# Kernel optimization log

Measured on AMD Instinct MI355X. Metric: run time of the kernel, lower is better.

## Reference

```python
import jax, jax.numpy as jnp
import numpy as np

B, L, ENC, DEC, ATT = 128, 196, 2048, 512, 512

def setup_inputs() -> dict:
    key = jax.random.key(0)
    ks = jax.random.split(key, 8)
    s_enc = 1.0 / np.sqrt(ENC)
    s_dec = 1.0 / np.sqrt(DEC)
    s_att = 1.0 / np.sqrt(ATT)
    return {
        "encoder_out": jax.random.normal(ks[0], (B, L, ENC), jnp.float32),
        "decoder_hidden": jax.random.normal(ks[1], (B, DEC), jnp.float32),
        "We": jax.random.uniform(ks[2], (ENC, ATT), jnp.float32, -s_enc, s_enc),
        "be": jax.random.uniform(ks[3], (ATT,), jnp.float32, -s_enc, s_enc),
        "Wd": jax.random.uniform(ks[4], (DEC, ATT), jnp.float32, -s_dec, s_dec),
        "bd": jax.random.uniform(ks[5], (ATT,), jnp.float32, -s_dec, s_dec),
        "wa": jax.random.uniform(ks[6], (ATT,), jnp.float32, -s_att, s_att),
        "ba": jax.random.uniform(ks[7], (), jnp.float32, -s_att, s_att),
    }

def reference(encoder_out, decoder_hidden, We, be, Wd, bd, wa, ba):
    # encoder_out: [B, L, ENC]; decoder_hidden: [B, DEC]
    enc_map = jnp.einsum('ble,ea->bla', encoder_out, We) + be          # [B, L, A]
    dec_map = decoder_hidden @ Wd + bd                                  # [B, A]
    scores = jnp.tanh(enc_map + dec_map[:, None, :]) @ wa + ba         # [B, L]
    alphas = jax.nn.softmax(scores, axis=1)                             # [B, L]
    context = jnp.einsum('bl,ble->be', alphas, encoder_out)             # [B, ENC]
    return (context, alphas)
```

## Files before the change

### kernel.cpp

```cpp
#include <hip/hip_runtime.h>

#define B_   128
#define L_   196
#define ENC_ 2048
#define DEC_ 512
#define ATT_ 512
#define M_   (B_ * L_)

typedef _Float16 f16x4 __attribute__((ext_vector_type(4)));
typedef _Float16 f16x8 __attribute__((ext_vector_type(8)));
typedef __fp16   h16x2 __attribute__((ext_vector_type(2)));
typedef float    f32x4 __attribute__((ext_vector_type(4)));

#define FENCE_LDS_BARRIER()                                        \
    do {                                                           \
        asm volatile("s_waitcnt lgkmcnt(0)" ::: "memory");         \
        __builtin_amdgcn_s_barrier();                              \
        __builtin_amdgcn_sched_barrier(0);                         \
    } while (0)


__global__ void wets_kernel(const float* __restrict__ We, _Float16* __restrict__ WeTs) {
    int u = blockIdx.x * 256 + threadIdx.x;
    int row = u & 127;
    int k8  = (u >> 7) & 3;
    int kt  = (u >> 9) & 63;
    int nt  = u >> 15;
    int n  = nt * 128 + row;
    int k0 = kt * 32 + k8 * 8;
    f16x8 h;
#pragma unroll
    for (int j = 0; j < 8; ++j) h[j] = (_Float16)We[(k0 + j) * ATT_ + n];
    *reinterpret_cast<f16x8*>(WeTs + (size_t)u * 8) = h;
}

__global__ void decmap_kernel(const float* __restrict__ dh, const float* __restrict__ Wd,
                              const float* __restrict__ bd, float* __restrict__ dec) {
    int b = blockIdx.x;
    int a = threadIdx.x;
    float acc = bd[a];
    const float* dhp = dh + b * DEC_;
#pragma unroll 8
    for (int k = 0; k < DEC_; ++k) acc += dhp[k] * Wd[k * ATT_ + a];
    dec[b * ATT_ + a] = acc;
}

__global__ __launch_bounds__(256, 3)
void gemm_score_kernel(const float* __restrict__ enc,
                       const _Float16* __restrict__ WeTs,
                       const float* __restrict__ be,
                       const float* __restrict__ wa,
                       const float* __restrict__ dec,
                       float* __restrict__ partial) {
    __shared__ _Float16 smem[2][2][4096];
    __shared__ float red[2][128];

    int bid = blockIdx.x;
    int sid = (bid & 7) * 98 + (bid >> 3);
    int mtile = sid >> 2;
    int ntile = sid & 3;

    int tid  = threadIdx.x;
    int lane = tid & 63, wid = tid >> 6;
    int wm = wid >> 1, wn = wid & 1;
    int l15 = lane & 15, lg = lane >> 4;

    int arowi = tid >> 2;
    int ac8   = tid & 3;
    const float* agA = enc + (size_t)(mtile * 128 + arowi) * ENC_ + ac8 * 8;
    const float* agB = agA + (size_t)64 * ENC_;
    int wa0 = (ac8 * 128 + (arowi ^ (2 * ac8))) * 8;
    int wa1 = wa0 + 64 * 8;

    const _Float16* bbase = WeTs + (size_t)ntile * 64 * 4096;

    int afo = (lg * 128 + wm * 64 + (l15 ^ (2 * lg))) * 8;
    int bfo = (lg * 128 + wn * 64 + l15) * 8;

    float4 areg0[4], areg1[4];
    f16x8  breg0[2], breg1[2];

    f32x4 acc[4][4];
#pragma unroll
    for (int mi = 0; mi < 4; ++mi)
#pragma unroll
        for (int ni = 0; ni < 4; ++ni) acc[mi][ni] = (f32x4){0.f, 0.f, 0.f, 0.f};

    auto load0 = [&](int kt) {
        const float* a0 = agA + kt * 32;
        const float* a1 = agB + kt * 32;
        areg0[0] = *reinterpret_cast<const float4*>(a0);
        areg0[1] = *reinterpret_cast<const float4*>(a0 + 4);
        areg0[2] = *reinterpret_cast<const float4*>(a1);
        areg0[3] = *reinterpret_cast<const float4*>(a1 + 4);
        const _Float16* bs = bbase + (size_t)kt * 4096;
        breg0[0] = *reinterpret_cast<const f16x8*>(bs + tid * 8);
        breg0[1] = *reinterpret_cast<const f16x8*>(bs + (tid + 256) * 8);
    };
    auto load1 = [&](int kt) {
        const float* a0 = agA + kt * 32;
        const float* a1 = agB + kt * 32;
        areg1[0] = *reinterpret_cast<const float4*>(a0);
        areg1[1] = *reinterpret_cast<const float4*>(a0 + 4);
        areg1[2] = *reinterpret_cast<const float4*>(a1);
        areg1[3] = *reinterpret_cast<const float4*>(a1 + 4);
        const _Float16* bs = bbase + (size_t)kt * 4096;
        breg1[0] = *reinterpret_cast<const f16x8*>(bs + tid * 8);
        breg1[1] = *reinterpret_cast<const f16x8*>(bs + (tid + 256) * 8);
    };
    auto write0 = [&](int buf) {
        _Float16* As = smem[buf][0];
        _Float16* Bs = smem[buf][1];
        union { h16x2 h2[4]; f16x8 h8; } cv;
        cv.h2[0] = __builtin_amdgcn_cvt_pkrtz(areg0[0].x, areg0[0].y);
        cv.h2[1] = __builtin_amdgcn_cvt_pkrtz(areg0[0].z, areg0[0].w);
        cv.h2[2] = __builtin_amdgcn_cvt_pkrtz(areg0[1].x, areg0[1].y);
        cv.h2[3] = __builtin_amdgcn_cvt_pkrtz(areg0[1].z, areg0[1].w);
        *reinterpret_cast<f16x8*>(As + wa0) = cv.h8;
        cv.h2[0] = __builtin_amdgcn_cvt_pkrtz(areg0[2].x, areg0[2].y);
        cv.h2[1] = __builtin_amdgcn_cvt_pkrtz(areg0[2].z, areg0[2].w);
        cv.h2[2] = __builtin_amdgcn_cvt_pkrtz(areg0[3].x, areg0[3].y);
        cv.h2[3] = __builtin_amdgcn_cvt_pkrtz(areg0[3].z, areg0[3].w);
        *reinterpret_cast<f16x8*>(As + wa1) = cv.h8;
        *reinterpret_cast<f16x8*>(Bs + tid * 8) = breg0[0];
        *reinterpret_cast<f16x8*>(Bs + (tid + 256) * 8) = breg0[1];
    };
    auto write1 = [&](int buf) {
        _Float16* As = smem[buf][0];
        _Float16* Bs = smem[buf][1];
        union { h16x2 h2[4]; f16x8 h8; } cv;
        cv.h2[0] = __builtin_amdgcn_cvt_pkrtz(areg1[0].x, areg1[0].y);
        cv.h2[1] = __builtin_amdgcn_cvt_pkrtz(areg1[0].z, areg1[0].w);
        cv.h2[2] = __builtin_amdgcn_cvt_pkrtz(areg1[1].x, areg1[1].y);
        cv.h2[3] = __builtin_amdgcn_cvt_pkrtz(areg1[1].z, areg1[1].w);
        *reinterpret_cast<f16x8*>(As + wa0) = cv.h8;
        cv.h2[0] = __builtin_amdgcn_cvt_pkrtz(areg1[2].x, areg1[2].y);
        cv.h2[1] = __builtin_amdgcn_cvt_pkrtz(areg1[2].z, areg1[2].w);
        cv.h2[2] = __builtin_amdgcn_cvt_pkrtz(areg1[3].x, areg1[3].y);
        cv.h2[3] = __builtin_amdgcn_cvt_pkrtz(areg1[3].z, areg1[3].w);
        *reinterpret_cast<f16x8*>(As + wa1) = cv.h8;
        *reinterpret_cast<f16x8*>(Bs + tid * 8) = breg1[0];
        *reinterpret_cast<f16x8*>(Bs + (tid + 256) * 8) = breg1[1];
    };
    auto compute = [&](const _Float16* As, const _Float16* Bs) {
        f16x8 af[4], bf[4];
#pragma unroll
        for (int mi = 0; mi < 4; ++mi)
            af[mi] = *reinterpret_cast<const f16x8*>(As + afo + mi * 128);
#pragma unroll
        for (int ni = 0; ni < 4; ++ni)
            bf[ni] = *reinterpret_cast<const f16x8*>(Bs + bfo + ni * 128);
#pragma unroll
        for (int mi = 0; mi < 4; ++mi)
#pragma unroll
            for (int ni = 0; ni < 4; ++ni)
                acc[mi][ni] = __builtin_amdgcn_mfma_f32_16x16x32_f16(
                    af[mi], bf[ni], acc[mi][ni], 0, 0, 0);
    };

    load0(0);
    load1(1);
    write0(0);
    FENCE_LDS_BARRIER();

    for (int kt2 = 0; kt2 < 32; ++kt2) {
        int kt = kt2 * 2;
        if (kt2 < 31) load0(kt + 2);
        compute(smem[0][0], smem[0][1]);
        write1(1);
        FENCE_LDS_BARRIER();
        if (kt2 < 31) load1(kt + 3);
        compute(smem[1][0], smem[1][1]);
        if (kt2 < 31) write0(0);
        FENCE_LDS_BARRIER();
    }

    float rsum[4][4];
#pragma unroll
    for (int mi = 0; mi < 4; ++mi)
#pragma unroll
        for (int j = 0; j < 4; ++j) rsum[mi][j] = 0.f;

    int nb = ntile * 128 + wn * 64;
    int rb = mtile * 128 + wm * 64;
#pragma unroll
    for (int ni = 0; ni < 4; ++ni) {
        int n = nb + ni * 16 + l15;
        float wav = wa[n];
        float bev = be[n];
#pragma unroll
        for (int mi = 0; mi < 4; ++mi) {
#pragma unroll
            for (int j = 0; j < 4; ++j) {
                int row = rb + mi * 16 + lg * 4 + j;
                int b = row / L_;
                float x = acc[mi][ni][j] + bev + dec[b * ATT_ + n];
                float e = __expf(2.0f * x);
                float t = 1.0f - 2.0f / (e + 1.0f);
                rsum[mi][j] += t * wav;
            }
        }
    }
#pragma unroll
    for (int mi = 0; mi < 4; ++mi) {
#pragma unroll
        for (int j = 0; j < 4; ++j) {
            float v = rsum[mi][j];
            v += __shfl_xor(v, 1);
            v += __shfl_xor(v, 2);
            v += __shfl_xor(v, 4);
            v += __shfl_xor(v, 8);
            if (l15 == 0) red[wn][wm * 64 + mi * 16 + lg * 4 + j] = v;
        }
    }
    __syncthreads();
    if (tid < 128)
        partial[(size_t)ntile * M_ + mtile * 128 + tid] = red[0][tid] + red[1][tid];
}

__global__ void softmax_kernel(const float* __restrict__ partial, float* __restrict__ alphas) {
    int b = blockIdx.x, t = threadIdx.x;
    int lane = t & 63, wid = t >> 6;
    __shared__ float red[4];
    float s = 0.f, val = -1e30f;
    if (t < L_) {
        int r = b * L_ + t;
        s = partial[r] + partial[M_ + r] + partial[2 * M_ + r] + partial[3 * M_ + r];
        val = s;
    }
    float m = val;
#pragma unroll
    for (int off = 1; off < 64; off <<= 1) m = fmaxf(m, __shfl_xor(m, off));
    if (lane == 0) red[wid] = m;
    __syncthreads();
    m = fmaxf(fmaxf(red[0], red[1]), fmaxf(red[2], red[3]));
    float e = (t < L_) ? __expf(s - m) : 0.f;
    float sum = e;
#pragma unroll
    for (int off = 1; off < 64; off <<= 1) sum += __shfl_xor(sum, off);
    __syncthreads();
    if (lane == 0) red[wid] = sum;
    __syncthreads();
    sum = red[0] + red[1] + red[2] + red[3];
    if (t < L_) alphas[b * L_ + t] = e / sum;
}

__global__ void context_kernel(const float* __restrict__ enc, const float* __restrict__ alphas,
                               float* __restrict__ ctx) {
    int b = blockIdx.x >> 2;
    int ec = blockIdx.x & 3;
    int e = ec * 512 + threadIdx.x * 2;
    const float* ep = enc + (size_t)b * L_ * ENC_ + e;
    const float* ap = alphas + b * L_;
    float ax = 0.f, ay = 0.f;
#pragma unroll 4
    for (int l = 0; l < L_; ++l) {
        float a = ap[l];
        float2 v = *reinterpret_cast<const float2*>(ep + (size_t)l * ENC_);
        ax += a * v.x;
        ay += a * v.y;
    }
    float2 r; r.x = ax; r.y = ay;
    *reinterpret_cast<float2*>(&ctx[b * ENC_ + e]) = r;
}

extern "C" void kernel_launch(void* const* d_in, const int* in_sizes, int n_in,
                              void* d_out, int out_size, void* d_ws, size_t ws_size,
                              hipStream_t stream) {
    const float* enc = (const float*)d_in[0];
    const float* dh  = (const float*)d_in[1];
    const float* We  = (const float*)d_in[2];
    const float* be  = (const float*)d_in[3];
    const float* Wd  = (const float*)d_in[4];
    const float* bd  = (const float*)d_in[5];
    const float* wa  = (const float*)d_in[6];

    float* out    = (float*)d_out;
    float* ctx    = out;
    float* alphas = out + B_ * ENC_;

    char* ws = (char*)d_ws;
    float*    dec     = (float*)ws;
    _Float16* WeTs    = (_Float16*)(ws + 262144);
    float*    partial = (float*)(ws + 262144 + 2097152);

    hipLaunchKernelGGL(wets_kernel,       dim3(512),  dim3(256), 0, stream, We, WeTs);
    hipLaunchKernelGGL(decmap_kernel,     dim3(128),  dim3(512), 0, stream, dh, Wd, bd, dec);
    hipLaunchKernelGGL(gemm_score_kernel, dim3(784),  dim3(256), 0, stream, enc, WeTs, be, wa, dec, partial);
    hipLaunchKernelGGL(softmax_kernel,    dim3(128),  dim3(256), 0, stream, partial, alphas);
    hipLaunchKernelGGL(context_kernel,    dim3(512),  dim3(256), 0, stream, enc, alphas, ctx);
}
```

Before: 150.5 us.

## Load B fragments directly from global into registers, bypassing LDS

```diff
diff --git a/kernel.cpp b/kernel.cpp
--- a/kernel.cpp
+++ b/kernel.cpp
@@ -52,7 +52,7 @@
                        const float* __restrict__ wa,
                        const float* __restrict__ dec,
                        float* __restrict__ partial) {
-    __shared__ _Float16 smem[2][2][4096];
+    __shared__ _Float16 smem[2][4096];
     __shared__ float red[2][128];
 
     int bid = blockIdx.x;
@@ -72,13 +72,13 @@
     int wa0 = (ac8 * 128 + (arowi ^ (2 * ac8))) * 8;
     int wa1 = wa0 + 64 * 8;
 
-    const _Float16* bbase = WeTs + (size_t)ntile * 64 * 4096;
+    const _Float16* bfr = WeTs +
+        ((size_t)ntile * 64 * 4 * 128 + (size_t)lg * 128 + wn * 64 + l15) * 8;
 
     int afo = (lg * 128 + wm * 64 + (l15 ^ (2 * lg))) * 8;
-    int bfo = (lg * 128 + wn * 64 + l15) * 8;
 
     float4 areg0[4], areg1[4];
-    f16x8  breg0[2], breg1[2];
+    f16x8  bA[4], bB[4];
 
     f32x4 acc[4][4];
 #pragma unroll
@@ -86,31 +86,36 @@
 #pragma unroll
         for (int ni = 0; ni < 4; ++ni) acc[mi][ni] = (f32x4){0.f, 0.f, 0.f, 0.f};
 
-    auto load0 = [&](int kt) {
+    auto loadA0 = [&](int kt) {
         const float* a0 = agA + kt * 32;
         const float* a1 = agB + kt * 32;
         areg0[0] = *reinterpret_cast<const float4*>(a0);
         areg0[1] = *reinterpret_cast<const float4*>(a0 + 4);
         areg0[2] = *reinterpret_cast<const float4*>(a1);
         areg0[3] = *reinterpret_cast<const float4*>(a1 + 4);
-        const _Float16* bs = bbase + (size_t)kt * 4096;
-        breg0[0] = *reinterpret_cast<const f16x8*>(bs + tid * 8);
-        breg0[1] = *reinterpret_cast<const f16x8*>(bs + (tid + 256) * 8);
-    };
-    auto load1 = [&](int kt) {
+    };
+    auto loadA1 = [&](int kt) {
         const float* a0 = agA + kt * 32;
         const float* a1 = agB + kt * 32;
         areg1[0] = *reinterpret_cast<const float4*>(a0);
         areg1[1] = *reinterpret_cast<const float4*>(a0 + 4);
         areg1[2] = *reinterpret_cast<const float4*>(a1);
         areg1[3] = *reinterpret_cast<const float4*>(a1 + 4);
-        const _Float16* bs = bbase + (size_t)kt * 4096;
-        breg1[0] = *reinterpret_cast<const f16x8*>(bs + tid * 8);
-        breg1[1] = *reinterpret_cast<const f16x8*>(bs + (tid + 256) * 8);
-    };
-    auto write0 = [&](int buf) {
-        _Float16* As = smem[buf][0];
-        _Float16* Bs = smem[buf][1];
+    };
+    auto loadBA = [&](int kt) {
+        const _Float16* s = bfr + (size_t)kt * 4096;
+#pragma unroll
+        for (int ni = 0; ni < 4; ++ni)
+            bA[ni] = *reinterpret_cast<const f16x8*>(s + ni * 16 * 8);
+    };
+    auto loadBB = [&](int kt) {
+        const _Float16* s = bfr + (size_t)kt * 4096;
+#pragma unroll
+        for (int ni = 0; ni < 4; ++ni)
+            bB[ni] = *reinterpret_cast<const f16x8*>(s + ni * 16 * 8);
+    };
+    auto writeA0 = [&](int buf) {
+        _Float16* As = smem[buf];
         union { h16x2 h2[4]; f16x8 h8; } cv;
         cv.h2[0] = __builtin_amdgcn_cvt_pkrtz(areg0[0].x, areg0[0].y);
         cv.h2[1] = __builtin_amdgcn_cvt_pkrtz(areg0[0].z, areg0[0].w);
@@ -122,12 +127,9 @@
         cv.h2[2] = __builtin_amdgcn_cvt_pkrtz(areg0[3].x, areg0[3].y);
         cv.h2[3] = __builtin_amdgcn_cvt_pkrtz(areg0[3].z, areg0[3].w);
         *reinterpret_cast<f16x8*>(As + wa1) = cv.h8;
-        *reinterpret_cast<f16x8*>(Bs + tid * 8) = breg0[0];
-        *reinterpret_cast<f16x8*>(Bs + (tid + 256) * 8) = breg0[1];
-    };
-    auto write1 = [&](int buf) {
-        _Float16* As = smem[buf][0];
-        _Float16* Bs = smem[buf][1];
+    };
+    auto writeA1 = [&](int buf) {
+        _Float16* As = smem[buf];
         union { h16x2 h2[4]; f16x8 h8; } cv;
         cv.h2[0] = __builtin_amdgcn_cvt_pkrtz(areg1[0].x, areg1[0].y);
         cv.h2[1] = __builtin_amdgcn_cvt_pkrtz(areg1[0].z, areg1[0].w);
@@ -139,39 +141,41 @@
         cv.h2[2] = __builtin_amdgcn_cvt_pkrtz(areg1[3].x, areg1[3].y);
         cv.h2[3] = __builtin_amdgcn_cvt_pkrtz(areg1[3].z, areg1[3].w);
         *reinterpret_cast<f16x8*>(As + wa1) = cv.h8;
-        *reinterpret_cast<f16x8*>(Bs + tid * 8) = breg1[0];
-        *reinterpret_cast<f16x8*>(Bs + (tid + 256) * 8) = breg1[1];
-    };
-    auto compute = [&](const _Float16* As, const _Float16* Bs) {
-        f16x8 af[4], bf[4];
+    };
+    auto computeA = [&](const _Float16* As, const f16x8* bf) {
+        f16x8 af[4];
 #pragma unroll
         for (int mi = 0; mi < 4; ++mi)
             af[mi] = *reinterpret_cast<const f16x8*>(As + afo + mi * 128);
-#pragma unroll
-        for (int ni = 0; ni < 4; ++ni)
-            bf[ni] = *reinterpret_cast<const f16x8*>(Bs + bfo + ni * 128);
+        __builtin_amdgcn_s_setprio(1);
 #pragma unroll
         for (int mi = 0; mi < 4; ++mi)
 #pragma unroll
             for (int ni = 0; ni < 4; ++ni)
                 acc[mi][ni] = __builtin_amdgcn_mfma_f32_16x16x32_f16(
                     af[mi], bf[ni], acc[mi][ni], 0, 0, 0);
-    };
-
-    load0(0);
-    load1(1);
-    write0(0);
+        __builtin_amdgcn_s_setprio(0);
+    };
+
+    loadA0(0);
+    loadA1(1);
+    loadBA(0);
+    writeA0(0);
     FENCE_LDS_BARRIER();
 
     for (int kt2 = 0; kt2 < 32; ++kt2) {
         int kt = kt2 * 2;
-        if (kt2 < 31) load0(kt + 2);
-        compute(smem[0][0], smem[0][1]);
-        write1(1);
+        if (kt2 < 31) loadA0(kt + 2);
+        loadBB(kt + 1);
+        computeA(smem[0], bA);
+        writeA1(1);
         FENCE_LDS_BARRIER();
-        if (kt2 < 31) load1(kt + 3);
-        compute(smem[1][0], smem[1][1]);
-        if (kt2 < 31) write0(0);
+        if (kt2 < 31) {
+            loadA1(kt + 3);
+            loadBA(kt + 2);
+        }
+        computeA(smem[1], bB);
+        if (kt2 < 31) writeA0(0);
         FENCE_LDS_BARRIER();
     }
 
```

New measurement: 152.8 us. About the same (+1.5%).

## Pre-convert encoder to fp16 and use direct-to-LDS loads in GEMM and context

Applied to the files above, without the earlier changes.

```diff
diff --git a/kernel.cpp b/kernel.cpp
--- a/kernel.cpp
+++ b/kernel.cpp
@@ -7,7 +7,7 @@
 #define ATT_ 512
 #define M_   (B_ * L_)
 
-typedef _Float16 f16x4 __attribute__((ext_vector_type(4)));
+typedef _Float16 f16x4v __attribute__((ext_vector_type(4)));
 typedef _Float16 f16x8 __attribute__((ext_vector_type(8)));
 typedef __fp16   h16x2 __attribute__((ext_vector_type(2)));
 typedef float    f32x4 __attribute__((ext_vector_type(4)));
@@ -19,6 +19,28 @@
         __builtin_amdgcn_sched_barrier(0);                         \
     } while (0)
 
+__device__ __forceinline__ void gload16(const _Float16* g, _Float16* l) {
+    __builtin_amdgcn_global_load_lds(
+        (const __attribute__((address_space(1))) void*)g,
+        (__attribute__((address_space(3))) void*)l, 16, 0, 0);
+}
+
+
+__global__ void enc16_kernel(const float* __restrict__ enc, _Float16* __restrict__ enc16) {
+    size_t i = ((size_t)blockIdx.x * 256 + threadIdx.x) * 8;
+    size_t stride = (size_t)gridDim.x * 256 * 8;
+    size_t total = (size_t)M_ * ENC_;
+    for (; i < total; i += stride) {
+        float4 a = *reinterpret_cast<const float4*>(enc + i);
+        float4 b = *reinterpret_cast<const float4*>(enc + i + 4);
+        union { h16x2 h2[4]; f16x8 h8; } cv;
+        cv.h2[0] = __builtin_amdgcn_cvt_pkrtz(a.x, a.y);
+        cv.h2[1] = __builtin_amdgcn_cvt_pkrtz(a.z, a.w);
+        cv.h2[2] = __builtin_amdgcn_cvt_pkrtz(b.x, b.y);
+        cv.h2[3] = __builtin_amdgcn_cvt_pkrtz(b.z, b.w);
+        *reinterpret_cast<f16x8*>(enc16 + i) = cv.h8;
+    }
+}
 
 __global__ void wets_kernel(const float* __restrict__ We, _Float16* __restrict__ WeTs) {
     int u = blockIdx.x * 256 + threadIdx.x;
@@ -45,13 +67,151 @@
     dec[b * ATT_ + a] = acc;
 }
 
+__global__ __launch_bounds__(256, 4)
+void gemm16_kernel(const _Float16* __restrict__ enc16,
+                   const _Float16* __restrict__ WeTs,
+                   const float* __restrict__ be,
+                   const float* __restrict__ wa,
+                   const float* __restrict__ dec,
+                   float* __restrict__ partial) {
+    __shared__ __align__(16) _Float16 As[2][4096];
+    __shared__ __align__(16) _Float16 Bs[2][4096];
+    __shared__ float red[2][128];
+
+    int bid = blockIdx.x;
+    int sid = (bid & 7) * 98 + (bid >> 3);
+    int mtile = sid >> 2;
+    int ntile = sid & 3;
+
+    int tid  = threadIdx.x;
+    int lane = tid & 63, wid = tid >> 6;
+    int wm = wid >> 1, wn = wid & 1;
+    int l15 = lane & 15, lg = lane >> 4;
+
+    int r0 = tid >> 2, s0 = tid & 3;
+    int k8d = s0 ^ ((r0 >> 1) & 3);
+    const _Float16* ag = enc16 + (size_t)(mtile * 128 + r0) * ENC_ + k8d * 8;
+    const _Float16* bg = WeTs + (size_t)ntile * 64 * 4096 + tid * 8;
+
+    int afo[4];
+#pragma unroll
+    for (int mi = 0; mi < 4; ++mi) {
+        int row = wm * 64 + mi * 16 + l15;
+        afo[mi] = (row * 4 + (lg ^ ((l15 >> 1) & 3))) * 8;
+    }
+    int bfo = (lg * 128 + wn * 64 + l15) * 8;
+
+    f32x4 acc[4][4];
+#pragma unroll
+    for (int mi = 0; mi < 4; ++mi)
+#pragma unroll
+        for (int ni = 0; ni < 4; ++ni) acc[mi][ni] = (f32x4){0.f, 0.f, 0.f, 0.f};
+
+    auto stage = [&](int buf, int kt) {
+        gload16(ag + kt * 32,               &As[buf][tid * 8]);
+        gload16(ag + (size_t)64 * ENC_ + kt * 32, &As[buf][tid * 8 + 2048]);
+        gload16(bg + (size_t)kt * 4096,        &Bs[buf][tid * 8]);
+        gload16(bg + (size_t)kt * 4096 + 2048, &Bs[buf][tid * 8 + 2048]);
+    };
+    auto compute = [&](int buf) {
+        f16x8 af[4], bf[4];
+#pragma unroll
+        for (int mi = 0; mi < 4; ++mi)
+            af[mi] = *reinterpret_cast<const f16x8*>(&As[buf][afo[mi]]);
+#pragma unroll
+        for (int ni = 0; ni < 4; ++ni)
+            bf[ni] = *reinterpret_cast<const f16x8*>(&Bs[buf][bfo + ni * 128]);
+        __builtin_amdgcn_s_setprio(1);
+#pragma unroll
+        for (int mi = 0; mi < 4; ++mi)
+#pragma unroll
+            for (int ni = 0; ni < 4; ++ni)
+                acc[mi][ni] = __builtin_amdgcn_mfma_f32_16x16x32_f16(
+                    af[mi], bf[ni], acc[mi][ni], 0, 0, 0);
+        __builtin_amdgcn_s_setprio(0);
+    };
+
+    stage(0, 0);
+    __syncthreads();
+    for (int kt = 0; kt < 64; ++kt) {
+        int cur = kt & 1;
+        if (kt < 63) stage(cur ^ 1, kt + 1);
+        compute(cur);
+        __syncthreads();
+    }
+
+    float rsum[4][4];
+#pragma unroll
+    for (int mi = 0; mi < 4; ++mi)
+#pragma unroll
+        for (int j = 0; j < 4; ++j) rsum[mi][j] = 0.f;
+
+    int nb = ntile * 128 + wn * 64;
+    int rb = mtile * 128 + wm * 64;
+#pragma unroll
+    for (int ni = 0; ni < 4; ++ni) {
+        int n = nb + ni * 16 + l15;
+        float wav = wa[n];
+        float bev = be[n];
+#pragma unroll
+        for (int mi = 0; mi < 4; ++mi) {
+#pragma unroll
+            for (int j = 0; j < 4; ++j) {
+                int row = rb + mi * 16 + lg * 4 + j;
+                int b = row / L_;
+                float x = acc[mi][ni][j] + bev + dec[b * ATT_ + n];
+                float e = __expf(2.0f * x);
+                float t = 1.0f - 2.0f / (e + 1.0f);
+                rsum[mi][j] += t * wav;
+            }
+        }
+    }
+#pragma unroll
+    for (int mi = 0; mi < 4; ++mi) {
+#pragma unroll
+        for (int j = 0; j < 4; ++j) {
+            float v = rsum[mi][j];
+            v += __shfl_xor(v, 1);
+            v += __shfl_xor(v, 2);
+            v += __shfl_xor(v, 4);
+            v += __shfl_xor(v, 8);
+            if (l15 == 0) red[wn][wm * 64 + mi * 16 + lg * 4 + j] = v;
+        }
+    }
+    __syncthreads();
+    if (tid < 128)
+        partial[(size_t)ntile * M_ + mtile * 128 + tid] = red[0][tid] + red[1][tid];
+}
+
+__global__ void context16_kernel(const _Float16* __restrict__ enc16,
+                                 const float* __restrict__ alphas,
+                                 float* __restrict__ ctx) {
+    int b = blockIdx.x >> 1;
+    int ec = blockIdx.x & 1;
+    int e = ec * 1024 + threadIdx.x * 4;
+    const _Float16* ep = enc16 + (size_t)b * L_ * ENC_ + e;
+    const float* ap = alphas + b * L_;
+    float a0 = 0.f, a1 = 0.f, a2 = 0.f, a3 = 0.f;
+#pragma unroll 4
+    for (int l = 0; l < L_; ++l) {
+        float a = ap[l];
+        f16x4v v = *reinterpret_cast<const f16x4v*>(ep + (size_t)l * ENC_);
+        a0 += a * (float)v[0];
+        a1 += a * (float)v[1];
+        a2 += a * (float)v[2];
+        a3 += a * (float)v[3];
+    }
+    float4 r; r.x = a0; r.y = a1; r.z = a2; r.w = a3;
+    *reinterpret_cast<float4*>(&ctx[b * ENC_ + e]) = r;
+}
+
 __global__ __launch_bounds__(256, 3)
-void gemm_score_kernel(const float* __restrict__ enc,
-                       const _Float16* __restrict__ WeTs,
-                       const float* __restrict__ be,
-                       const float* __restrict__ wa,
-                       const float* __restrict__ dec,
-                       float* __restrict__ partial) {
+void gemm_r8_kernel(const float* __restrict__ enc,
+                    const _Float16* __restrict__ WeTs,
+                    const float* __restrict__ be,
+                    const float* __restrict__ wa,
+                    const float* __restrict__ dec,
+                    float* __restrict__ partial) {
     __shared__ _Float16 smem[2][2][4096];
     __shared__ float red[2][128];
 
@@ -73,7 +233,6 @@
     int wa1 = wa0 + 64 * 8;
 
     const _Float16* bbase = WeTs + (size_t)ntile * 64 * 4096;
-
     int afo = (lg * 128 + wm * 64 + (l15 ^ (2 * lg))) * 8;
     int bfo = (lg * 128 + wn * 64 + l15) * 8;
 
@@ -282,11 +441,24 @@
     char* ws = (char*)d_ws;
     float*    dec     = (float*)ws;
     _Float16* WeTs    = (_Float16*)(ws + 262144);
-    float*    partial = (float*)(ws + 262144 + 2097152);
-
-    hipLaunchKernelGGL(wets_kernel,       dim3(512),  dim3(256), 0, stream, We, WeTs);
-    hipLaunchKernelGGL(decmap_kernel,     dim3(128),  dim3(512), 0, stream, dh, Wd, bd, dec);
-    hipLaunchKernelGGL(gemm_score_kernel, dim3(784),  dim3(256), 0, stream, enc, WeTs, be, wa, dec, partial);
-    hipLaunchKernelGGL(softmax_kernel,    dim3(128),  dim3(256), 0, stream, partial, alphas);
-    hipLaunchKernelGGL(context_kernel,    dim3(512),  dim3(256), 0, stream, enc, alphas, ctx);
-}
+    float*    partial = (float*)(ws + 2359296);
+    _Float16* enc16   = (_Float16*)(ws + 4194304);
+
+    const size_t needA = 4194304ull + (size_t)M_ * ENC_ * 2;
+
+    hipLaunchKernelGGL(wets_kernel,   dim3(512), dim3(256), 0, stream, We, WeTs);
+    hipLaunchKernelGGL(decmap_kernel, dim3(128), dim3(512), 0, stream, dh, Wd, bd, dec);
+
+    if (ws_size >= needA) {
+        hipLaunchKernelGGL(enc16_kernel,    dim3(4096), dim3(256), 0, stream, enc, enc16);
+        hipLaunchKernelGGL(gemm16_kernel,   dim3(784),  dim3(256), 0, stream,
+                           enc16, WeTs, be, wa, dec, partial);
+        hipLaunchKernelGGL(softmax_kernel,  dim3(128),  dim3(256), 0, stream, partial, alphas);
+        hipLaunchKernelGGL(context16_kernel,dim3(256),  dim3(256), 0, stream, enc16, alphas, ctx);
+    } else {
+        hipLaunchKernelGGL(gemm_r8_kernel,  dim3(784),  dim3(256), 0, stream,
+                           enc, WeTs, be, wa, dec, partial);
+        hipLaunchKernelGGL(softmax_kernel,  dim3(128),  dim3(256), 0, stream, partial, alphas);
+        hipLaunchKernelGGL(context_kernel,  dim3(512),  dim3(256), 0, stream, enc, alphas, ctx);
+    }
+}
```

Measured after the change: 200.6 us. 33.3% more time.
